# Kernel tuning notes

Measured on AMD Instinct MI355X. Metric: run time of the kernel, lower is better.

Reference implementation:

```python
import jax, jax.numpy as jnp
import numpy as np
import math

NH = 16
SIGMA = 1.5
KS = 7


def _gaussian_blur_16x16(x):
    # x: (N, 16, 16); torchvision GaussianBlur(7, 1.5) with reflect padding
    hx = jnp.arange(KS, dtype=x.dtype) - (KS - 1) / 2.0
    k1 = jnp.exp(-0.5 * (hx / SIGMA) ** 2)
    k1 = k1 / k1.sum()
    k2 = jnp.outer(k1, k1)[None, None]  # (1,1,7,7)
    pad = KS // 2
    xp = jnp.pad(x, ((0, 0), (pad, pad), (pad, pad)), mode='reflect')[:, None]
    y = jax.lax.conv_general_dilated(xp, k2, (1, 1), 'VALID')
    return y[:, 0]


def _normalize(w):
    mn, mx = w.min(), w.max()
    return (w - mn) / (mx - mn)


def _blurred_map(f, b_perm):
    # f, b_perm: (B, 256, 256)
    B = f.shape[0]
    bi = f * b_perm
    bi = bi.reshape(B * 256, 16, 16)
    bl = _gaussian_blur_16x16(bi)
    bl = jnp.clip(_normalize(bl), 0.0, 1.0)
    bl = bl.reshape(B, 256, 256)
    return bl * f * b_perm


def setup_inputs() -> dict:
    key = jax.random.key(0)
    ks = jax.random.split(key, 16)
    B, T, C = 4, 827, 1024
    inp = {
        'x': jax.random.normal(ks[0], (B, T, C), jnp.float32),
        'h': jax.random.normal(ks[1], (B, NH, 827, 827), jnp.float32) * 0.1,
        'f01': jax.random.uniform(ks[2], (B, 256, 256), jnp.float32),
        'f02': jax.random.uniform(ks[3], (B, 256, 256), jnp.float32),
        'f12': jax.random.uniform(ks[4], (B, 256, 256), jnp.float32),
        'b01': jax.random.uniform(ks[5], (B, 256, 256), jnp.float32),
        'b02': jax.random.uniform(ks[6], (B, 256, 256), jnp.float32),
        'b12': jax.random.uniform(ks[7], (B, 256, 256), jnp.float32),
        'Wq': jax.random.normal(ks[8], (C, C), jnp.float32) * 0.02,
        'bq': jnp.zeros((C,), jnp.float32),
        'Wk': jax.random.normal(ks[9], (C, C), jnp.float32) * 0.02,
        'bk': jnp.zeros((C,), jnp.float32),
        'Wv': jax.random.normal(ks[10], (C, C), jnp.float32) * 0.02,
        'bv': jnp.zeros((C,), jnp.float32),
        'Wp': jax.random.normal(ks[11], (C, C), jnp.float32) * 0.02,
        'bp': jnp.zeros((C,), jnp.float32),
    }
    return inp


def reference(x, h, f01, f02, f12, b01, b02, b12,
              Wq, bq, Wk, bk, Wv, bv, Wp, bp):
    B, T, C = x.shape
    hd = C // NH
    # QKV projections -> (B, NH, T, hd)
    def proj(W, b):
        return (x @ W + b).reshape(B, T, NH, hd).transpose(0, 2, 1, 3)
    q, k, v = proj(Wq, bq), proj(Wk, bk), proj(Wv, bv)

    att = jnp.einsum('bhtd,bhsd->bhts', q, k) * (1.0 / math.sqrt(hd))
    att = h[:, :, :T, :T] + att  # adaptive additive bias

    # bidirectional epipolar multiplicative masks with blur
    b01p = jnp.transpose(b01, (0, 2, 1))
    b02p = jnp.transpose(b02, (0, 2, 1))
    b12p = jnp.transpose(b12, (0, 2, 1))
    blur01 = _blurred_map(f01, b01p)[:, None]  # (B,1,256,256), broadcast over heads
    blur02 = _blurred_map(f02, b02p)[:, None]
    blur12 = _blurred_map(f12, b12p)[:, None]

    n1 = min(T - 285, 256)
    att = att.at[:, :, 285:285 + n1, 0:256].multiply(blur01[:, :, :n1])
    if T > 571:
        n2 = T - 571
        att = att.at[:, :, 571:T, 0:256].multiply(blur02[:, :, :n2])
        att = att.at[:, :, 571:T, 286:542].multiply(blur12[:, :, :n2])

    mask = jnp.tril(jnp.ones((T, T), dtype=bool))
    att = jnp.where(mask, att, -jnp.inf)
    att = jax.nn.softmax(att, axis=-1)

    y = jnp.einsum('bhts,bhsd->bhtd', att, v)
    y = y.transpose(0, 2, 1, 3).reshape(B, T, C)
    return y @ Wp + bp
```

## Files before the change

kernel.cpp:

```cpp
#include <hip/hip_runtime.h>
#include <math.h>

using bfrag8 = __attribute__((ext_vector_type(8))) short;
using facc4  = __attribute__((ext_vector_type(4))) float;

#define MFMA16(a,b,c) __builtin_amdgcn_mfma_f32_16x16x32_bf16((a),(b),(c),0,0,0)

#define T_SEQ 827
#define T_PAD 832
#define NHEAD 16
#define NEG_INF (-__builtin_inff())
#define CM_TOT 1179392

static __device__ __forceinline__ unsigned short f2bf(float f) {
    unsigned int x = __float_as_uint(f);
    unsigned int r = x + 0x7FFFu + ((x >> 16) & 1u);
    return (unsigned short)(r >> 16);
}

static __device__ __forceinline__ void gl16(const unsigned short* g, unsigned short* l) {
    __builtin_amdgcn_global_load_lds(
        (const __attribute__((address_space(1))) unsigned int*)g,
        (__attribute__((address_space(3))) unsigned int*)l,
        16, 0, 0);
}

__global__ __launch_bounds__(256) void k_front(const float* __restrict__ x,
                                               unsigned short* __restrict__ x_bf,
                                               float* __restrict__ cm,
                                               unsigned short* q, unsigned short* k,
                                               unsigned short* vT,
                                               const float* __restrict__ Wq,
                                               const float* __restrict__ Wk,
                                               const float* __restrict__ Wv,
                                               const float* __restrict__ Wp,
                                               unsigned short* __restrict__ Wt_out,
                                               const float* f01, const float* f02, const float* f12,
                                               const float* b01, const float* b02, const float* b12,
                                               float* __restrict__ bl,
                                               float* __restrict__ pmm) {
    __shared__ float tile[32][33];
    __shared__ float img[16][17], tmp[16][17];
    __shared__ float smn[4], smx[4];
    int bid = blockIdx.x, tid = threadIdx.x;

    if (bid < 3308) {
        int i = (bid * 256 + tid) * 4;
        float4 v = *reinterpret_cast<const float4*>(x + i);
        ushort4 o;
        o.x = f2bf(v.x); o.y = f2bf(v.y); o.z = f2bf(v.z); o.w = f2bf(v.w);
        *reinterpret_cast<ushort4*>(x_bf + i) = o;
    } else if (bid < 4460) {
        int base = (bid - 3308) * 1024 + tid * 4;
        if (base + 4 <= CM_TOT) {
            float4 one = {1.f, 1.f, 1.f, 1.f};
            *reinterpret_cast<float4*>(cm + base) = one;
        } else {
#pragma unroll
            for (int j = 0; j < 4; ++j)
                if (base + j < CM_TOT) cm[base + j] = 1.f;
        }
    } else if (bid < 4524) {
        int bh = bid - 4460;
        for (int i = tid; i < 320; i += 256) {
            int t = 827 + i / 64, d = i % 64;
            q[((size_t)bh * T_PAD + t) * 64 + d] = 0;
            k[((size_t)bh * T_PAD + t) * 64 + d] = 0;
        }
        for (int i = tid; i < 4096; i += 256) {
            int d = i >> 6, s = 768 + (i & 63);
            vT[((size_t)bh * 64 + d) * T_PAD + s] = 0;
        }
    } else if (bid < 8620) {
        int i = bid - 4524;
        int z = i >> 10, rem = i & 1023;
        int bx = rem & 31, by = rem >> 5;
        const float* W = (z == 0) ? Wq : (z == 1) ? Wk : (z == 2) ? Wv : Wp;
        unsigned short* Wt = Wt_out + (size_t)z * 1048576;
        int tx = tid & 31, ty0 = tid >> 5;
#pragma unroll
        for (int j = 0; j < 4; ++j) {
            int ty = ty0 + j * 8;
            tile[ty][tx] = W[(size_t)(by * 32 + ty) * 1024 + bx * 32 + tx];
        }
        __syncthreads();
#pragma unroll
        for (int j = 0; j < 4; ++j) {
            int ty = ty0 + j * 8;
            Wt[(size_t)(bx * 32 + ty) * 1024 + by * 32 + tx] = f2bf(tile[tx][ty]);
        }
    } else {
        int i = bid - 8620;
        int m = i >> 10, rem = i & 1023, b = rem >> 8, r = rem & 255;
        const float* f  = (m == 0) ? f01 : (m == 1) ? f02 : f12;
        const float* bm = (m == 0) ? b01 : (m == 1) ? b02 : b12;
        int ii = tid >> 4, j = tid & 15;

        float k1[7]; float ks = 0.f;
#pragma unroll
        for (int d = 0; d < 7; ++d) { float hx = (float)d - 3.f; k1[d] = expf(-0.5f * hx * hx / 2.25f); ks += k1[d]; }
#pragma unroll
        for (int d = 0; d < 7; ++d) k1[d] /= ks;

        size_t idx = (size_t)b * 65536 + (size_t)r * 256 + tid;
        float bi = f[idx] * bm[(size_t)b * 65536 + (size_t)tid * 256 + r];
        img[ii][j] = bi;
        __syncthreads();
        float ha = 0.f;
#pragma unroll
        for (int d = 0; d < 7; ++d) { int p = j - 3 + d; p = p < 0 ? -p : (p > 15 ? 30 - p : p); ha += k1[d] * img[ii][p]; }
        tmp[ii][j] = ha;
        __syncthreads();
        float v = 0.f;
#pragma unroll
        for (int d = 0; d < 7; ++d) { int p = ii - 3 + d; p = p < 0 ? -p : (p > 15 ? 30 - p : p); v += k1[d] * tmp[p][j]; }
        bl[(size_t)m * 262144 + idx] = v;

        float mn = v, mx = v;
#pragma unroll
        for (int off = 32; off; off >>= 1) { mn = fminf(mn, __shfl_xor(mn, off)); mx = fmaxf(mx, __shfl_xor(mx, off)); }
        int wid = tid >> 6, lane = tid & 63;
        if (lane == 0) { smn[wid] = mn; smx[wid] = mx; }
        __syncthreads();
        if (tid == 0) {
            mn = fminf(fminf(smn[0], smn[1]), fminf(smn[2], smn[3]));
            mx = fmaxf(fmaxf(smx[0], smx[1]), fmaxf(smx[2], smx[3]));
            pmm[2 * i]     = mn;
            pmm[2 * i + 1] = mx;
        }
    }
}

__global__ __launch_bounds__(256) void k_reduce6(const float* __restrict__ pmm,
                                                 float* __restrict__ minmax) {
    int m = blockIdx.x, tid = threadIdx.x;
    float mn = __builtin_inff(), mx = 0.f;
    for (int k = tid; k < 1024; k += 256) {
        int e = m * 1024 + k;
        mn = fminf(mn, pmm[2 * e]);
        mx = fmaxf(mx, pmm[2 * e + 1]);
    }
#pragma unroll
    for (int off = 32; off; off >>= 1) { mn = fminf(mn, __shfl_xor(mn, off)); mx = fmaxf(mx, __shfl_xor(mx, off)); }
    __shared__ float smn[4], smx[4];
    int wid = tid >> 6, lane = tid & 63;
    if (lane == 0) { smn[wid] = mn; smx[wid] = mx; }
    __syncthreads();
    if (tid == 0) {
        mn = fminf(fminf(smn[0], smn[1]), fminf(smn[2], smn[3]));
        mx = fmaxf(fmaxf(smx[0], smx[1]), fmaxf(smx[2], smx[3]));
        minmax[2 * m] = mn; minmax[2 * m + 1] = mx;
    }
}

__global__ __launch_bounds__(256) void k_finalize(const float* f01, const float* f02, const float* f12,
                                                  const float* b01, const float* b02, const float* b12,
                                                  const float* __restrict__ bl, const float* minmax,
                                                  float* __restrict__ cm) {
    int m = blockIdx.x >> 10, rem = blockIdx.x & 1023, b = rem >> 8, r = rem & 255;
    const float* f  = (m == 0) ? f01 : (m == 1) ? f02 : f12;
    const float* bm = (m == 0) ? b01 : (m == 1) ? b02 : b12;
    int tid = threadIdx.x;
    size_t idx = (size_t)b * 65536 + (size_t)r * 256 + tid;
    float mn = minmax[2 * m], mx = minmax[2 * m + 1];
    float w = (bl[(size_t)m * 262144 + idx] - mn) / (mx - mn);
    w = fminf(fmaxf(w, 0.f), 1.f);
    float val = w * f[idx] * bm[(size_t)b * 65536 + (size_t)tid * 256 + r];
    int row = (m == 0) ? r : r + 286;
    int col = (m == 2) ? tid + 286 : tid;
    cm[((size_t)b * 542 + row) * 544 + col] = val;
}

template<int MODE>
__global__ __launch_bounds__(256) void k_gemm(const unsigned short* __restrict__ A,
                                              const unsigned short* __restrict__ Bt,
                                              const float* __restrict__ b0, const float* __restrict__ b1,
                                              const float* __restrict__ b2,
                                              unsigned short* __restrict__ qo, unsigned short* __restrict__ ko,
                                              unsigned short* __restrict__ vo, float* __restrict__ fo, int M) {
    __shared__ unsigned short As[4096];
    __shared__ unsigned short Bs[4096];
    int m0 = blockIdx.x * 128, n0 = blockIdx.y * 128;
    int tid = threadIdx.x, wid = tid >> 6, lane = tid & 63;
    int g = lane >> 4, l15 = lane & 15;
    int wm = wid >> 1, wn = wid & 1;
    facc4 acc[4][4] = {};

    int ar0 = m0 + (tid >> 2); if (ar0 > M - 1) ar0 = M - 1;
    int ar1 = m0 + 64 + (tid >> 2); if (ar1 > M - 1) ar1 = M - 1;
    const unsigned short* Ap0 = A + (size_t)ar0 * 1024 + (tid & 3) * 8;
    const unsigned short* Ap1 = A + (size_t)ar1 * 1024 + (tid & 3) * 8;
    const unsigned short* Bp0 = Bt + (size_t)(n0 + (tid >> 2)) * 1024 + (tid & 3) * 8;
    const unsigned short* Bp1 = Bp0 + (size_t)64 * 1024;
    unsigned short* asw = As + (wid << 9);
    unsigned short* bsw = Bs + (wid << 9);

    for (int k0 = 0; k0 < 1024; k0 += 32) {
        if (k0) __syncthreads();
        gl16(Ap0 + k0, asw);
        gl16(Ap1 + k0, asw + 2048);
        gl16(Bp0 + k0, bsw);
        gl16(Bp1 + k0, bsw + 2048);
        __syncthreads();
        bfrag8 af[4], bf[4];
#pragma unroll
        for (int mi = 0; mi < 4; ++mi)
            af[mi] = *reinterpret_cast<const bfrag8*>(&As[(wm * 64 + mi * 16 + l15) * 32 + g * 8]);
#pragma unroll
        for (int ni = 0; ni < 4; ++ni)
            bf[ni] = *reinterpret_cast<const bfrag8*>(&Bs[(wn * 64 + ni * 16 + l15) * 32 + g * 8]);
#pragma unroll
        for (int mi = 0; mi < 4; ++mi)
#pragma unroll
            for (int ni = 0; ni < 4; ++ni)
                acc[mi][ni] = MFMA16(af[mi], bf[ni], acc[mi][ni]);
    }

    int which = n0 >> 10;
    const float* bb = (MODE == 2) ? b0 : (which == 0 ? b0 : (which == 1 ? b1 : b2));
#pragma unroll
    for (int mi = 0; mi < 4; ++mi)
#pragma unroll
        for (int ni = 0; ni < 4; ++ni)
#pragma unroll
            for (int r = 0; r < 4; ++r) {
                int row = m0 + wm * 64 + mi * 16 + g * 4 + r;
                if (row >= M) continue;
                int col = n0 + wn * 64 + ni * 16 + l15;
                float v = acc[mi][ni][r] + bb[col & 1023];
                if (MODE == 2) {
                    fo[(size_t)row * 1024 + col] = v;
                } else {
                    int b = row / T_SEQ, t = row - b * T_SEQ;
                    int cc = col & 1023;
                    int hh = cc >> 6, d = cc & 63;
                    size_t bh = (size_t)(b * NHEAD + hh);
                    if (which == 0) {
                        qo[(bh * T_PAD + t) * 64 + d] = f2bf(v);
                    } else if (which == 1) {
                        int du = (((d >> 3) ^ (t & 7)) << 3) | (d & 7);
                        ko[(bh * T_PAD + t) * 64 + du] = f2bf(v);
                    } else {
                        int sl = t & 63;
                        int su = (((sl >> 3) ^ (d & 7)) << 3) | (t & 7);
                        vo[(bh * 64 + d) * T_PAD + (t - sl) + su] = f2bf(v);
                    }
                }
            }
}

__global__ __launch_bounds__(256) void k_attn(const unsigned short* __restrict__ qb,
                                              const unsigned short* __restrict__ kb,
                                              const unsigned short* __restrict__ vT,
                                              const float* __restrict__ h,
                                              const float* __restrict__ cm,
                                              unsigned short* __restrict__ y) {
    int blk = blockIdx.x;
    int bh = blk / 13;
    int qt = 12 - (blk % 13);
    int b = bh >> 4, hh = bh & 15;
    int tid = threadIdx.x, wid = tid >> 6, lane = tid & 63;
    int g = lane >> 4, l15 = lane & 15;
    int t0 = qt * 64 + wid * 16;
    int t = t0 + l15;
    int tcl = t > 826 ? 826 : t;
    int ntiles = qt + 1;

    __shared__ unsigned short Ks[2][4096];
    __shared__ unsigned short Vs[2][4096];
    __shared__ unsigned short Ps[4][1024];
    unsigned short* pw = &Ps[wid][0];

    const unsigned short* Kbase = kb + (size_t)bh * T_PAD * 64;
    const unsigned short* Vbase = vT + (size_t)bh * 64 * T_PAD;
    const float* hrow = h + (size_t)bh * T_SEQ * T_SEQ + (size_t)tcl * T_SEQ;
    int rt = t - 285; rt = rt < 0 ? 0 : (rt > 541 ? 541 : rt);
    const float* cmrow = cm + ((size_t)b * 542 + rt) * 544;
    bool tm = (t >= 285);

    size_t qrow = ((size_t)bh * T_PAD + t) * 64 + g * 8;
    bfrag8 aq0 = *reinterpret_cast<const bfrag8*>(qb + qrow);
    bfrag8 aq1 = *reinterpret_cast<const bfrag8*>(qb + qrow + 32);

    auto stage = [&](int s0, int buf) {
        const unsigned short* kt = Kbase + (size_t)s0 * 64;
        unsigned short* kd = &Ks[buf][0] + (wid << 9);
        gl16(kt + tid * 8, kd);
        gl16(kt + 2048 + tid * 8, kd + 2048);
        const unsigned short* vt = Vbase + s0;
        unsigned short* vd = &Vs[buf][0] + (wid << 9);
        gl16(vt + (size_t)(tid >> 3) * T_PAD + (tid & 7) * 8, vd);
        gl16(vt + (size_t)((tid >> 3) + 32) * T_PAD + (tid & 7) * 8, vd + 2048);
    };

    auto loadh = [&](int s0t, float* hv, float* mv) {
#pragma unroll
        for (int nt = 0; nt < 4; ++nt) {
            int sb = s0t + nt * 16 + 4 * g;
            float h4[4];
            if (sb + 3 <= tcl) {
                __builtin_memcpy(h4, hrow + sb, 16);
            } else {
#pragma unroll
                for (int j = 0; j < 4; ++j) {
                    float hx = 0.f;
                    if (sb + j <= tcl) hx = hrow[sb + j];
                    h4[j] = hx;
                }
            }
            float m4[4];
            if (tm && sb <= 540) {
                __builtin_memcpy(m4, cmrow + sb, 16);
            } else {
#pragma unroll
                for (int j = 0; j < 4; ++j) m4[j] = 1.f;
            }
#pragma unroll
            for (int j = 0; j < 4; ++j) { hv[nt * 4 + j] = h4[j]; mv[nt * 4 + j] = m4[j]; }
        }
    };

    float m_r = NEG_INF, l_r = 0.f;
    facc4 acc[4] = {};
    float hv[16], mv[16];
    loadh(0, hv, mv);
    stage(0, 0);

    for (int it = 0; it < ntiles; ++it) {
        int cur = it & 1, s0 = it * 64;
        bool more = (it + 1 < ntiles);
        bool diag = !more;
        __syncthreads();
        if (more) stage(s0 + 64, cur ^ 1);

        facc4 sf[4] = {};
        __builtin_amdgcn_s_setprio(1);
#pragma unroll
        for (int nt = 0; nt < 4; ++nt) {
            int row = nt * 16 + l15;
            const unsigned short* kp = &Ks[cur][row * 64];
            bfrag8 k0 = *reinterpret_cast<const bfrag8*>(kp + ((g ^ (row & 7)) << 3));
            bfrag8 k1 = *reinterpret_cast<const bfrag8*>(kp + (((4 + g) ^ (row & 7)) << 3));
            sf[nt] = MFMA16(k0, aq0, sf[nt]);
            sf[nt] = MFMA16(k1, aq1, sf[nt]);
        }
        __builtin_amdgcn_s_setprio(0);

        float vmax = NEG_INF;
#pragma unroll
        for (int nt = 0; nt < 4; ++nt)
#pragma unroll
            for (int r = 0; r < 4; ++r) {
                float val = fmaf(sf[nt][r], 0.125f, hv[nt * 4 + r]) * mv[nt * 4 + r];
                if (diag) {
                    int s = s0 + nt * 16 + 4 * g + r;
                    val = (s <= tcl) ? val : NEG_INF;
                }
                sf[nt][r] = val;
                vmax = fmaxf(vmax, val);
            }

        if (more) loadh(s0 + 64, hv, mv);

        vmax = fmaxf(vmax, __shfl_xor(vmax, 16));
        vmax = fmaxf(vmax, __shfl_xor(vmax, 32));
        float mnew = fmaxf(m_r, vmax);

        float ps = 0.f;
#pragma unroll
        for (int nt = 0; nt < 4; ++nt)
#pragma unroll
            for (int r = 0; r < 4; ++r) {
                float p = __expf(sf[nt][r] - mnew);
                sf[nt][r] = p;
                ps += p;
            }
        ps += __shfl_xor(ps, 16);
        ps += __shfl_xor(ps, 32);

#pragma unroll
        for (int nt = 0; nt < 4; ++nt) {
            unsigned u0, u1;
            asm("v_cvt_pk_bf16_f32 %0, %1, %2" : "=v"(u0) : "v"(sf[nt][0]), "v"(sf[nt][1]));
            asm("v_cvt_pk_bf16_f32 %0, %1, %2" : "=v"(u1) : "v"(sf[nt][2]), "v"(sf[nt][3]));
            int el = (l15 * 64 + nt * 16 + 4 * g) ^ ((l15 & 7) << 3);
            uint2 uu; uu.x = u0; uu.y = u1;
            *reinterpret_cast<uint2*>(&pw[el]) = uu;
        }

        if (__any(mnew > m_r)) {
            float scale = __expf(m_r - mnew);
            l_r = l_r * scale + ps;
#pragma unroll
            for (int r = 0; r < 4; ++r) {
                float sc = __int_as_float(__builtin_amdgcn_ds_bpermute((4 * g + r) * 4, __float_as_int(scale)));
#pragma unroll
                for (int dt = 0; dt < 4; ++dt) acc[dt][r] *= sc;
            }
        } else {
            l_r += ps;
        }
        m_r = mnew;

        __builtin_amdgcn_s_setprio(1);
#pragma unroll
        for (int c2 = 0; c2 < 2; ++c2) {
            int ela = (l15 * 64 + c2 * 32 + 8 * g) ^ ((l15 & 7) << 3);
            bfrag8 ap = *reinterpret_cast<const bfrag8*>(&pw[ela]);
#pragma unroll
            for (int dt = 0; dt < 4; ++dt) {
                int row = dt * 16 + l15;
                bfrag8 vf = *reinterpret_cast<const bfrag8*>(&Vs[cur][row * 64 + (((c2 * 4 + g) ^ (row & 7)) << 3)]);
                acc[dt] = MFMA16(ap, vf, acc[dt]);
            }
        }
        __builtin_amdgcn_s_setprio(0);
    }

    float linv = 1.0f / l_r;
#pragma unroll
    for (int r = 0; r < 4; ++r) {
        float li = __int_as_float(__builtin_amdgcn_ds_bpermute((4 * g + r) * 4, __float_as_int(linv)));
        int tt = t0 + 4 * g + r;
        if (tt < T_SEQ) {
#pragma unroll
            for (int dt = 0; dt < 4; ++dt)
                y[((size_t)(b * T_SEQ) + tt) * 1024 + hh * 64 + dt * 16 + l15] = f2bf(acc[dt][r] * li);
        }
    }
}

extern "C" void kernel_launch(void* const* d_in, const int* in_sizes, int n_in,
                              void* d_out, int out_size, void* d_ws, size_t ws_size,
                              hipStream_t stream) {
    const float* x   = (const float*)d_in[0];
    const float* h   = (const float*)d_in[1];
    const float* f01 = (const float*)d_in[2];
    const float* f02 = (const float*)d_in[3];
    const float* f12 = (const float*)d_in[4];
    const float* b01 = (const float*)d_in[5];
    const float* b02 = (const float*)d_in[6];
    const float* b12 = (const float*)d_in[7];
    const float* Wq  = (const float*)d_in[8];
    const float* bq  = (const float*)d_in[9];
    const float* Wk  = (const float*)d_in[10];
    const float* bk  = (const float*)d_in[11];
    const float* Wv  = (const float*)d_in[12];
    const float* bv  = (const float*)d_in[13];
    const float* Wp  = (const float*)d_in[14];
    const float* bp  = (const float*)d_in[15];

    char* ws = (char*)d_ws;
    float* minmax = (float*)ws;
    float* pmm    = (float*)(ws + 256);
    float* bl     = (float*)(ws + 256 + 24576);
    float* cmb    = (float*)(ws + 256 + 24576 + 3145728);
    unsigned short* x_bf  = (unsigned short*)(ws + 256 + 24576 + 3145728 + 4717568);
    unsigned short* WtQKV = x_bf + (size_t)3308 * 1024;
    unsigned short* WtP   = WtQKV + (size_t)3072 * 1024;
    unsigned short* q_bf  = WtP + (size_t)1024 * 1024;
    unsigned short* k_bf  = q_bf + (size_t)64 * T_PAD * 64;
    unsigned short* vTb   = k_bf + (size_t)64 * T_PAD * 64;
    unsigned short* y_bf  = vTb  + (size_t)64 * T_PAD * 64;

    k_front<<<11692, 256, 0, stream>>>(x, x_bf, cmb, q_bf, k_bf, vTb,
                                       Wq, Wk, Wv, Wp, WtQKV,
                                       f01, f02, f12, b01, b02, b12, bl, pmm);
    k_reduce6<<<3, 256, 0, stream>>>(pmm, minmax);
    k_finalize<<<3072, 256, 0, stream>>>(f01, f02, f12, b01, b02, b12, bl, minmax, cmb);

    dim3 gqkv(26, 24);
    k_gemm<0><<<gqkv, 256, 0, stream>>>(x_bf, WtQKV, bq, bk, bv, q_bf, k_bf, vTb, nullptr, 3308);
    k_attn<<<832, 256, 0, stream>>>(q_bf, k_bf, vTb, h, cmb, y_bf);
    dim3 gp(26, 8);
    k_gemm<2><<<gp, 256, 0, stream>>>(y_bf, WtP, bp, nullptr, nullptr, nullptr, nullptr, nullptr,
                                      (float*)d_out, 3308);
}
```

Baseline: 153.1 us.

## Fuse mask finalize into QKV GEMM, XCD-swizzle blocks, lazy softmax rescale

Drops the separate min/max reduce and finalize kernels. Their work now runs as extra blocks appended to the QKV GEMM launch, and each of those blocks recomputes the per-mask min/max from the partials. GEMM and attention block indices are remapped so neighbouring tiles land on the same XCD, aiming for better L2 reuse. Online softmax skips rescaling the accumulator unless the running max grows by more than a threshold, which cuts exp and multiply work at the cost of possible loss of precision and overflow headroom.

```diff
diff --git a/kernel.cpp b/kernel.cpp
--- a/kernel.cpp
+++ b/kernel.cpp
@@ -131,57 +131,61 @@
     }
 }
 
-__global__ __launch_bounds__(256) void k_reduce6(const float* __restrict__ pmm,
-                                                 float* __restrict__ minmax) {
-    int m = blockIdx.x, tid = threadIdx.x;
-    float mn = __builtin_inff(), mx = 0.f;
-    for (int k = tid; k < 1024; k += 256) {
-        int e = m * 1024 + k;
-        mn = fminf(mn, pmm[2 * e]);
-        mx = fmaxf(mx, pmm[2 * e + 1]);
-    }
-#pragma unroll
-    for (int off = 32; off; off >>= 1) { mn = fminf(mn, __shfl_xor(mn, off)); mx = fmaxf(mx, __shfl_xor(mx, off)); }
-    __shared__ float smn[4], smx[4];
-    int wid = tid >> 6, lane = tid & 63;
-    if (lane == 0) { smn[wid] = mn; smx[wid] = mx; }
-    __syncthreads();
-    if (tid == 0) {
-        mn = fminf(fminf(smn[0], smn[1]), fminf(smn[2], smn[3]));
-        mx = fmaxf(fmaxf(smx[0], smx[1]), fmaxf(smx[2], smx[3]));
-        minmax[2 * m] = mn; minmax[2 * m + 1] = mx;
-    }
-}
-
-__global__ __launch_bounds__(256) void k_finalize(const float* f01, const float* f02, const float* f12,
-                                                  const float* b01, const float* b02, const float* b12,
-                                                  const float* __restrict__ bl, const float* minmax,
-                                                  float* __restrict__ cm) {
-    int m = blockIdx.x >> 10, rem = blockIdx.x & 1023, b = rem >> 8, r = rem & 255;
-    const float* f  = (m == 0) ? f01 : (m == 1) ? f02 : f12;
-    const float* bm = (m == 0) ? b01 : (m == 1) ? b02 : b12;
-    int tid = threadIdx.x;
-    size_t idx = (size_t)b * 65536 + (size_t)r * 256 + tid;
-    float mn = minmax[2 * m], mx = minmax[2 * m + 1];
-    float w = (bl[(size_t)m * 262144 + idx] - mn) / (mx - mn);
-    w = fminf(fmaxf(w, 0.f), 1.f);
-    float val = w * f[idx] * bm[(size_t)b * 65536 + (size_t)tid * 256 + r];
-    int row = (m == 0) ? r : r + 286;
-    int col = (m == 2) ? tid + 286 : tid;
-    cm[((size_t)b * 542 + row) * 544 + col] = val;
-}
-
 template<int MODE>
 __global__ __launch_bounds__(256) void k_gemm(const unsigned short* __restrict__ A,
                                               const unsigned short* __restrict__ Bt,
                                               const float* __restrict__ b0, const float* __restrict__ b1,
                                               const float* __restrict__ b2,
                                               unsigned short* __restrict__ qo, unsigned short* __restrict__ ko,
-                                              unsigned short* __restrict__ vo, float* __restrict__ fo, int M) {
+                                              unsigned short* __restrict__ vo, float* __restrict__ fo, int M,
+                                              const float* f01, const float* f02, const float* f12,
+                                              const float* b01, const float* b02, const float* b12,
+                                              const float* __restrict__ bl,
+                                              const float* __restrict__ pmm,
+                                              float* __restrict__ cm) {
     __shared__ unsigned short As[4096];
     __shared__ unsigned short Bs[4096];
-    int m0 = blockIdx.x * 128, n0 = blockIdx.y * 128;
-    int tid = threadIdx.x, wid = tid >> 6, lane = tid & 63;
+    int bid = blockIdx.x, tid = threadIdx.x;
+
+    if (MODE == 0 && bid >= 624) {
+        int i = bid - 624;
+        int m = i >> 10, rem = i & 1023, b = rem >> 8, r = rem & 255;
+        float mn = __builtin_inff(), mx = 0.f;
+        for (int kk = tid; kk < 1024; kk += 256) {
+            int e = m * 1024 + kk;
+            mn = fminf(mn, pmm[2 * e]);
+            mx = fmaxf(mx, pmm[2 * e + 1]);
+        }
+#pragma unroll
+        for (int off = 32; off; off >>= 1) { mn = fminf(mn, __shfl_xor(mn, off)); mx = fmaxf(mx, __shfl_xor(mx, off)); }
+        float* fs = reinterpret_cast<float*>(As);
+        int wid = tid >> 6, lane = tid & 63;
+        if (lane == 0) { fs[wid] = mn; fs[4 + wid] = mx; }
+        __syncthreads();
+        mn = fminf(fminf(fs[0], fs[1]), fminf(fs[2], fs[3]));
+        mx = fmaxf(fmaxf(fs[4], fs[5]), fmaxf(fs[6], fs[7]));
+
+        const float* f  = (m == 0) ? f01 : (m == 1) ? f02 : f12;
+        const float* bm = (m == 0) ? b01 : (m == 1) ? b02 : b12;
+        size_t idx = (size_t)b * 65536 + (size_t)r * 256 + tid;
+        float w = (bl[(size_t)m * 262144 + idx] - mn) / (mx - mn);
+        w = fminf(fmaxf(w, 0.f), 1.f);
+        float val = w * f[idx] * bm[(size_t)b * 65536 + (size_t)tid * 256 + r];
+        int row = (m == 0) ? r : r + 286;
+        int col = (m == 2) ? tid + 286 : tid;
+        cm[((size_t)b * 542 + row) * 544 + col] = val;
+        return;
+    }
+
+    int m0, n0;
+    if (MODE == 0) {
+        int swz = (bid & 7) * 78 + (bid >> 3);
+        m0 = (swz % 26) * 128; n0 = (swz / 26) * 128;
+    } else {
+        int swz = (bid & 7) * 26 + (bid >> 3);
+        m0 = (swz % 26) * 128; n0 = (swz / 26) * 128;
+    }
+    int wid = tid >> 6, lane = tid & 63;
     int g = lane >> 4, l15 = lane & 15;
     int wm = wid >> 1, wn = wid & 1;
     facc4 acc[4][4] = {};
@@ -255,7 +259,8 @@
                                               const float* __restrict__ h,
                                               const float* __restrict__ cm,
                                               unsigned short* __restrict__ y) {
-    int blk = blockIdx.x;
+    int blk0 = blockIdx.x;
+    int blk = (blk0 & 7) * 104 + (blk0 >> 3);
     int bh = blk / 13;
     int qt = 12 - (blk % 13);
     int b = bh >> 4, hh = bh & 15;
@@ -364,14 +369,17 @@
 
         vmax = fmaxf(vmax, __shfl_xor(vmax, 16));
         vmax = fmaxf(vmax, __shfl_xor(vmax, 32));
+
+        bool noresc = __all(vmax <= m_r + 6.0f);
         float mnew = fmaxf(m_r, vmax);
+        float mexp = noresc ? m_r : mnew;
 
         float ps = 0.f;
 #pragma unroll
         for (int nt = 0; nt < 4; ++nt)
 #pragma unroll
             for (int r = 0; r < 4; ++r) {
-                float p = __expf(sf[nt][r] - mnew);
+                float p = __expf(sf[nt][r] - mexp);
                 sf[nt][r] = p;
                 ps += p;
             }
@@ -388,7 +396,7 @@
             *reinterpret_cast<uint2*>(&pw[el]) = uu;
         }
 
-        if (__any(mnew > m_r)) {
+        if (!noresc) {
             float scale = __expf(m_r - mnew);
             l_r = l_r * scale + ps;
 #pragma unroll
@@ -397,10 +405,10 @@
 #pragma unroll
                 for (int dt = 0; dt < 4; ++dt) acc[dt][r] *= sc;
             }
+            m_r = mnew;
         } else {
             l_r += ps;
         }
-        m_r = mnew;
 
         __builtin_amdgcn_s_setprio(1);
 #pragma unroll
@@ -451,7 +459,6 @@
     const float* bp  = (const float*)d_in[15];
 
     char* ws = (char*)d_ws;
-    float* minmax = (float*)ws;
     float* pmm    = (float*)(ws + 256);
     float* bl     = (float*)(ws + 256 + 24576);
     float* cmb    = (float*)(ws + 256 + 24576 + 3145728);
@@ -466,13 +473,11 @@
     k_front<<<11692, 256, 0, stream>>>(x, x_bf, cmb, q_bf, k_bf, vTb,
                                        Wq, Wk, Wv, Wp, WtQKV,
                                        f01, f02, f12, b01, b02, b12, bl, pmm);
-    k_reduce6<<<3, 256, 0, stream>>>(pmm, minmax);
-    k_finalize<<<3072, 256, 0, stream>>>(f01, f02, f12, b01, b02, b12, bl, minmax, cmb);
-
-    dim3 gqkv(26, 24);
-    k_gemm<0><<<gqkv, 256, 0, stream>>>(x_bf, WtQKV, bq, bk, bv, q_bf, k_bf, vTb, nullptr, 3308);
+    k_gemm<0><<<3696, 256, 0, stream>>>(x_bf, WtQKV, bq, bk, bv, q_bf, k_bf, vTb, nullptr, 3308,
+                                        f01, f02, f12, b01, b02, b12, bl, pmm, cmb);
     k_attn<<<832, 256, 0, stream>>>(q_bf, k_bf, vTb, h, cmb, y_bf);
-    dim3 gp(26, 8);
-    k_gemm<2><<<gp, 256, 0, stream>>>(y_bf, WtP, bp, nullptr, nullptr, nullptr, nullptr, nullptr,
-                                      (float*)d_out, 3308);
-}
+    k_gemm<2><<<208, 256, 0, stream>>>(y_bf, WtP, bp, nullptr, nullptr, nullptr, nullptr, nullptr,
+                                       (float*)d_out, 3308,
+                                       nullptr, nullptr, nullptr, nullptr, nullptr, nullptr,
+                                       nullptr, nullptr, nullptr);
+}
```

After: 142.7 us. -6.8%, faster.
